# Performance work log

Measured on AMD Instinct MI355X. Metric: run time of the kernel, lower is better.

The kernel has to match this reference:

```python
import jax, jax.numpy as jnp
import numpy as np

B, C, H, W = 64, 512, 32, 32
D = C // 8  # 64


def setup_inputs() -> dict:
    key = jax.random.key(0)
    k1, k2, k3, k4 = jax.random.split(key, 4)
    x = jax.random.normal(k1, (B, C, H, W), dtype=jnp.float32)
    query_m = jax.random.normal(k2, (H * W, D), dtype=jnp.float32)
    key_m = jax.random.normal(k3, (H * W, D), dtype=jnp.float32)
    # 1x1 conv C->C: weight [C_out, C_in], kaiming-ish scale
    value_w = jax.random.normal(k4, (C, C), dtype=jnp.float32) * (1.0 / np.sqrt(C))
    value_b = jnp.zeros((C,), dtype=jnp.float32)
    return {"x": x, "query_m": query_m, "key_m": key_m,
            "value_w": value_w, "value_b": value_b}


def reference(x, query_m, key_m, value_w, value_b):
    b, c, h, w = x.shape
    xf = x.reshape(b, c, h * w)                        # [B, C, N]
    q = jnp.einsum('bcn,nd->bcd', xf, query_m)         # [B, C, D]
    k = jnp.einsum('bcn,nd->bcd', xf, key_m)           # [B, C, D]
    energy = jnp.einsum('bcd,bed->bce', q, k)          # [B, C, C]
    energy = jax.nn.sigmoid(energy)
    attention = jax.nn.softmax(energy, axis=-2)        # softmax over rows (dim=-2)
    # 1x1 conv = channel matmul + bias
    v = jnp.einsum('bcn,oc->bon', xf, value_w) + value_b[None, :, None]  # [B, C, N]
    # out[b,j,n] = sum_i v[b,i,n] * attention[b,i,j]
    out = jnp.einsum('bin,bij->bjn', v, attention)     # [B, C, N]
    return out.reshape(b, c, h, w)
```

## Files before the change

kernel.cpp:

```cpp
#include <hip/hip_runtime.h>

#define BK 32

typedef __attribute__((ext_vector_type(8))) short bf16x8;
typedef __attribute__((ext_vector_type(4))) float f32x4;

__device__ __forceinline__ unsigned short f2bf(float f) {
  unsigned u = __builtin_bit_cast(unsigned, f);
  unsigned r = (u + 0x7FFFu + ((u >> 16) & 1u)) >> 16;
  return (unsigned short)r;
}
__device__ __forceinline__ float bf2f(unsigned short h) {
  return __builtin_bit_cast(float, (unsigned)h << 16);
}
__device__ __forceinline__ unsigned pack2(unsigned short a, unsigned short b) {
  return (unsigned)a | ((unsigned)b << 16);
}

__device__ __forceinline__ void gld_lds16(const void* g, void* l) {
  __builtin_amdgcn_global_load_lds(
      (const __attribute__((address_space(1))) unsigned int*)g,
      (__attribute__((address_space(3))) unsigned int*)l, 16, 0, 0);
}

#define SCHED0() __builtin_amdgcn_sched_barrier(0)
#define NTBAR() do { SCHED0(); __builtin_amdgcn_s_barrier(); SCHED0(); } while (0)
#define VMW(N) do { asm volatile("s_waitcnt vmcnt(" #N ")" ::: "memory"); SCHED0(); } while (0)
#define LGKM0() do { asm volatile("s_waitcnt lgkmcnt(0)" ::: "memory"); SCHED0(); } while (0)
#define MFMA16(a, b, c) __builtin_amdgcn_mfma_f32_16x16x32_bf16(a, b, c, 0, 0, 0)

__device__ __forceinline__ void split8_store(float4 v0, float4 v1,
                                             unsigned short* Hdst,
                                             unsigned short* Ldst) {
  float f[8] = {v0.x, v0.y, v0.z, v0.w, v1.x, v1.y, v1.z, v1.w};
  unsigned short hh[8], ll[8];
#pragma unroll
  for (int i = 0; i < 8; ++i) {
    hh[i] = f2bf(f[i]);
    ll[i] = f2bf(f[i] - bf2f(hh[i]));
  }
  *reinterpret_cast<uint4*>(Hdst) = make_uint4(pack2(hh[0], hh[1]), pack2(hh[2], hh[3]),
                                               pack2(hh[4], hh[5]), pack2(hh[6], hh[7]));
  *reinterpret_cast<uint4*>(Ldst) = make_uint4(pack2(ll[0], ll[1]), pack2(ll[2], ll[3]),
                                               pack2(ll[4], ll[5]), pack2(ll[6], ll[7]));
}

__device__ __forceinline__ void split8_store_tt(float4 v0, float4 v1,
                                                unsigned short* Hdst,
                                                unsigned short* Ldst,
                                                unsigned short* Ttb,
                                                int kslot, int c) {
  float f[8] = {v0.x, v0.y, v0.z, v0.w, v1.x, v1.y, v1.z, v1.w};
  unsigned short hh[8], ll[8];
#pragma unroll
  for (int i = 0; i < 8; ++i) {
    hh[i] = f2bf(f[i]);
    ll[i] = f2bf(f[i] - bf2f(hh[i]));
  }
  *reinterpret_cast<uint4*>(Hdst) = make_uint4(pack2(hh[0], hh[1]), pack2(hh[2], hh[3]),
                                               pack2(hh[4], hh[5]), pack2(hh[6], hh[7]));
  *reinterpret_cast<uint4*>(Ldst) = make_uint4(pack2(ll[0], ll[1]), pack2(ll[2], ll[3]),
                                               pack2(ll[4], ll[5]), pack2(ll[6], ll[7]));
#pragma unroll
  for (int i = 0; i < 8; ++i) {
    int g = ((c >> 3) ^ i ^ kslot) & 7;
    Ttb[(kslot * 8 + i) * 72 + g * 8 + (c & 7)] = hh[i];
  }
}

__global__ __launch_bounds__(256) void qkm_split(const float* __restrict__ Qm,
                                                 const float* __restrict__ Km,
                                                 unsigned short* __restrict__ Th,
                                                 unsigned short* __restrict__ Tl) {
  __shared__ float lt[64][65];
  int k0 = blockIdx.x * 64;
  int half = blockIdx.y;
  const float* M = half ? Km : Qm;
  int t = threadIdx.x;
  int cl = (t & 15) * 4;
  int rl = t >> 4;
#pragma unroll
  for (int rr = 0; rr < 4; ++rr) {
    int r = rl + rr * 16;
    float4 v = *reinterpret_cast<const float4*>(&M[(long)(k0 + r) * 64 + cl]);
    lt[cl + 0][r] = v.x;
    lt[cl + 1][r] = v.y;
    lt[cl + 2][r] = v.z;
    lt[cl + 3][r] = v.w;
  }
  __syncthreads();
#pragma unroll
  for (int rr = 0; rr < 4; ++rr) {
    int c = rl + rr * 16;
    unsigned short h[4], lo[4];
#pragma unroll
    for (int i = 0; i < 4; ++i) {
      float f = lt[c][cl + i];
      h[i] = f2bf(f);
      lo[i] = f2bf(f - bf2f(h[i]));
    }
    *reinterpret_cast<uint2*>(&Th[(long)(half * 64 + c) * 1024 + k0 + cl]) =
        make_uint2(pack2(h[0], h[1]), pack2(h[2], h[3]));
    *reinterpret_cast<uint2*>(&Tl[(long)(half * 64 + c) * 1024 + k0 + cl]) =
        make_uint2(pack2(lo[0], lo[1]), pack2(lo[2], lo[3]));
  }
}

__global__ __launch_bounds__(256) void k1_mfma(const float* __restrict__ x,
                                               const unsigned short* __restrict__ Th,
                                               const unsigned short* __restrict__ Tl,
                                               unsigned short* __restrict__ qkh,
                                               unsigned short* __restrict__ qkl,
                                               unsigned short* __restrict__ xbT) {
  __shared__ unsigned short Dh[2][128 * 32];
  __shared__ unsigned short Dl[2][128 * 32];
  __shared__ unsigned short Xh[2][64 * 32];
  __shared__ unsigned short Xl[2][64 * 32];
  __shared__ unsigned short Tt[2][32 * 72];
  const int t = threadIdx.x;
  const int l = t & 63;
  const int w = t >> 6;
  const int wr = w >> 1, wc = w & 1;
  const long mBase = (long)blockIdx.x * 64;
  const int b = blockIdx.x >> 3;
  const int cBase = (blockIdx.x & 7) * 64;

  f32x4 acc[4][2];
#pragma unroll
  for (int m = 0; m < 4; ++m)
#pragma unroll
    for (int n = 0; n < 2; ++n) acc[m][n] = (f32x4){0.f, 0.f, 0.f, 0.f};

  const int xrow_l = t >> 2;
  const int kslot = t & 3;
  const int xsl = kslot ^ ((t >> 3) & 3);
  const int srcslot = (l & 3) ^ ((l >> 3) & 3);
  const int frag_off = (l & 15) * 32 + ((((l >> 4) ^ (l >> 1)) & 3) * 8);
  const float* xrow = x + (mBase + xrow_l) * 1024;

#define K1_STAGE_B(k0, p)                                                     \
  {                                                                           \
    _Pragma("unroll") for (int c = 0; c < 2; ++c) {                           \
      int ch = c * 4 + w;                                                     \
      int row = ch * 16 + (l >> 2);                                           \
      gld_lds16(Th + (long)row * 1024 + (k0) + srcslot * 8, &Dh[p][ch * 512]);\
      gld_lds16(Tl + (long)row * 1024 + (k0) + srcslot * 8, &Dl[p][ch * 512]);\
    }                                                                         \
  }

#define K1_COMPUTE(p)                                                         \
  {                                                                           \
    bf16x8 dh[4], dl[4], xh[2], xl[2];                                        \
    _Pragma("unroll") for (int m = 0; m < 4; ++m) {                           \
      dh[m] = *reinterpret_cast<const bf16x8*>(&Dh[p][(wr * 64 + m * 16) * 32 + frag_off]); \
      dl[m] = *reinterpret_cast<const bf16x8*>(&Dl[p][(wr * 64 + m * 16) * 32 + frag_off]); \
    }                                                                         \
    _Pragma("unroll") for (int n = 0; n < 2; ++n) {                           \
      xh[n] = *reinterpret_cast<const bf16x8*>(&Xh[p][(wc * 32 + n * 16) * 32 + frag_off]); \
      xl[n] = *reinterpret_cast<const bf16x8*>(&Xl[p][(wc * 32 + n * 16) * 32 + frag_off]); \
    }                                                                         \
    _Pragma("unroll") for (int m = 0; m < 4; ++m)                             \
        _Pragma("unroll") for (int n = 0; n < 2; ++n) {                       \
      acc[m][n] = MFMA16(dh[m], xh[n], acc[m][n]);                            \
      acc[m][n] = MFMA16(dh[m], xl[n], acc[m][n]);                            \
      acc[m][n] = MFMA16(dl[m], xh[n], acc[m][n]);                            \
    }                                                                         \
  }

#define K1_WRITEBACK(p, kk)                                                   \
  {                                                                           \
    int n2 = t >> 3;                                                          \
    int g2 = t & 7;                                                           \
    int gs = (g2 ^ (n2 & 7) ^ (n2 >> 3)) & 7;                                 \
    uint4 vv = *reinterpret_cast<const uint4*>(&Tt[p][n2 * 72 + gs * 8]);     \
    *reinterpret_cast<uint4*>(                                                \
        &xbT[(long)b * 524288 + (long)((kk) + n2) * 512 + cBase + g2 * 8]) = vv; \
  }

  {
    float4 p0 = *reinterpret_cast<const float4*>(&xrow[kslot * 8]);
    float4 p1 = *reinterpret_cast<const float4*>(&xrow[kslot * 8 + 4]);
    K1_STAGE_B(0, 0);
    split8_store_tt(p0, p1, &Xh[0][xrow_l * 32 + xsl * 8], &Xl[0][xrow_l * 32 + xsl * 8],
                    Tt[0], kslot, xrow_l);
  }

  for (int k0 = 0; k0 < 1024; k0 += 64) {
    __syncthreads();
    float4 na0 = *reinterpret_cast<const float4*>(&xrow[k0 + 32 + kslot * 8]);
    float4 na1 = *reinterpret_cast<const float4*>(&xrow[k0 + 32 + kslot * 8 + 4]);
    K1_STAGE_B(k0 + 32, 1);
    K1_COMPUTE(0);
    split8_store_tt(na0, na1, &Xh[1][xrow_l * 32 + xsl * 8], &Xl[1][xrow_l * 32 + xsl * 8],
                    Tt[1], kslot, xrow_l);
    K1_WRITEBACK(0, k0);
    __syncthreads();
    if (k0 + 64 < 1024) {
      float4 nb0 = *reinterpret_cast<const float4*>(&xrow[k0 + 64 + kslot * 8]);
      float4 nb1 = *reinterpret_cast<const float4*>(&xrow[k0 + 64 + kslot * 8 + 4]);
      K1_STAGE_B(k0 + 64, 0);
      K1_COMPUTE(1);
      split8_store_tt(nb0, nb1, &Xh[0][xrow_l * 32 + xsl * 8], &Xl[0][xrow_l * 32 + xsl * 8],
                      Tt[0], kslot, xrow_l);
      K1_WRITEBACK(1, k0 + 32);
    } else {
      K1_COMPUTE(1);
      K1_WRITEBACK(1, k0 + 32);
    }
  }

#pragma unroll
  for (int m = 0; m < 4; ++m)
#pragma unroll
    for (int n = 0; n < 2; ++n) {
      int d0 = wr * 64 + m * 16 + (l >> 4) * 4;
      long xr = mBase + wc * 32 + n * 16 + (l & 15);
      unsigned short h4[4], l4[4];
#pragma unroll
      for (int reg = 0; reg < 4; ++reg) {
        float v = acc[m][n][reg];
        h4[reg] = f2bf(v);
        l4[reg] = f2bf(v - bf2f(h4[reg]));
      }
      *reinterpret_cast<uint2*>(&qkh[xr * 128 + d0]) =
          make_uint2(pack2(h4[0], h4[1]), pack2(h4[2], h4[3]));
      *reinterpret_cast<uint2*>(&qkl[xr * 128 + d0]) =
          make_uint2(pack2(l4[0], l4[1]), pack2(l4[2], l4[3]));
    }
#undef K1_STAGE_B
#undef K1_COMPUTE
#undef K1_WRITEBACK
}

__global__ __launch_bounds__(256) void k2a_mfma(const unsigned short* __restrict__ qkh,
                                                const unsigned short* __restrict__ qkl,
                                                unsigned short* __restrict__ st) {
  __shared__ unsigned short Ah[128 * 64];
  __shared__ unsigned short Al[128 * 64];
  __shared__ unsigned short Bh[128 * 64];
  __shared__ unsigned short Bl[128 * 64];
  const int t = threadIdx.x;
  const int l = t & 63;
  const int w = t >> 6;
  const int wr = w >> 1, wc = w & 1;

  const int cpx = gridDim.x >> 3;
  const int orig = blockIdx.x;
  const int lw = (orig & 7) * cpx + (orig >> 3);
  const int b = lw >> 4;
  const int tile = lw & 15;
  const int iBase = (tile >> 2) * 128;
  const int jBase = (tile & 3) * 128;
  const long bq = (long)b * 512;

  const int sg = (l & 7) ^ (l >> 3);
#pragma unroll
  for (int c4 = 0; c4 < 4; ++c4) {
    int rb = w * 32 + c4 * 8;
    long rowA = bq + iBase + rb + (l >> 3);
    long rowB = bq + jBase + rb + (l >> 3);
    gld_lds16(qkh + rowA * 128 + sg * 8, &Ah[rb * 64]);
    gld_lds16(qkl + rowA * 128 + sg * 8, &Al[rb * 64]);
    gld_lds16(qkh + rowB * 128 + 64 + sg * 8, &Bh[rb * 64]);
    gld_lds16(qkl + rowB * 128 + 64 + sg * 8, &Bl[rb * 64]);
  }
  __syncthreads();

  f32x4 acc[4][4];
#pragma unroll
  for (int m = 0; m < 4; ++m)
#pragma unroll
    for (int n = 0; n < 4; ++n) acc[m][n] = (f32x4){0.f, 0.f, 0.f, 0.f};

#pragma unroll
  for (int ks = 0; ks < 2; ++ks) {
    bf16x8 ah[4], al4[4], bh[4], bl4[4];
#pragma unroll
    for (int m = 0; m < 4; ++m) {
      int row = wr * 64 + m * 16 + (l & 15);
      int off = row * 64 + ((ks * 4 + (l >> 4)) ^ (row & 7)) * 8;
      ah[m] = *reinterpret_cast<const bf16x8*>(&Ah[off]);
      al4[m] = *reinterpret_cast<const bf16x8*>(&Al[off]);
    }
#pragma unroll
    for (int n = 0; n < 4; ++n) {
      int row = wc * 64 + n * 16 + (l & 15);
      int off = row * 64 + ((ks * 4 + (l >> 4)) ^ (row & 7)) * 8;
      bh[n] = *reinterpret_cast<const bf16x8*>(&Bh[off]);
      bl4[n] = *reinterpret_cast<const bf16x8*>(&Bl[off]);
    }
#pragma unroll
    for (int m = 0; m < 4; ++m)
#pragma unroll
      for (int n = 0; n < 4; ++n) {
        acc[m][n] = MFMA16(ah[m], bh[n], acc[m][n]);
        acc[m][n] = MFMA16(ah[m], bl4[n], acc[m][n]);
        acc[m][n] = MFMA16(al4[m], bh[n], acc[m][n]);
      }
  }

  unsigned short* sb = st + (long)b * 512 * 512;
#pragma unroll
  for (int m = 0; m < 4; ++m)
#pragma unroll
    for (int n = 0; n < 4; ++n) {
      int i0 = iBase + wr * 64 + m * 16 + (l >> 4) * 4;
      int j = jBase + wc * 64 + n * 16 + (l & 15);
      unsigned short p[4];
#pragma unroll
      for (int reg = 0; reg < 4; ++reg) {
        float sg2 = 1.0f / (1.0f + __expf(-acc[m][n][reg]));
        p[reg] = f2bf(__expf(sg2));
      }
      *reinterpret_cast<uint2*>(&sb[(long)j * 512 + i0]) = *reinterpret_cast<uint2*>(p);
    }
}

__global__ __launch_bounds__(256) void k2b_rsum(const unsigned short* __restrict__ st,
                                                const float* __restrict__ bias,
                                                float* __restrict__ rsum,
                                                float* __restrict__ attbias) {
  int jg = blockIdx.x * 4 + (threadIdx.x >> 6);
  int l = threadIdx.x & 63;
  const unsigned short* row = st + (long)jg * 512 + l * 8;
  ushort4 u0 = *reinterpret_cast<const ushort4*>(row);
  ushort4 u1 = *reinterpret_cast<const ushort4*>(row + 4);
  float4 b0 = *reinterpret_cast<const float4*>(&bias[l * 8]);
  float4 b1 = *reinterpret_cast<const float4*>(&bias[l * 8 + 4]);
  float f0 = bf2f(u0.x), f1 = bf2f(u0.y), f2 = bf2f(u0.z), f3 = bf2f(u0.w);
  float f4 = bf2f(u1.x), f5 = bf2f(u1.y), f6 = bf2f(u1.z), f7 = bf2f(u1.w);
  float sum = (f0 + f1) + (f2 + f3) + ((f4 + f5) + (f6 + f7));
  float sumb = f0 * b0.x + f1 * b0.y + f2 * b0.z + f3 * b0.w +
               f4 * b1.x + f5 * b1.y + f6 * b1.z + f7 * b1.w;
#pragma unroll
  for (int off = 32; off > 0; off >>= 1) {
    sum += __shfl_down(sum, off);
    sumb += __shfl_down(sumb, off);
  }
  if (l == 0) {
    float r = 1.0f / sum;
    rsum[jg] = r;
    attbias[jg] = sumb * r;
  }
}

__global__ __launch_bounds__(256) void transpose_conv(const float* __restrict__ in,
                                                      unsigned short* __restrict__ out,
                                                      int inRows, int inCols,
                                                      long inBatch, long outBatch) {
  __shared__ unsigned short lt[64][65];
  int b = blockIdx.z;
  int r0 = blockIdx.y * 64;
  int c0 = blockIdx.x * 64;
  const float* I = in + (long)b * inBatch;
  unsigned short* O = out + (long)b * outBatch;
  int t = threadIdx.x;
  int cl = (t & 15) * 4;
  int rl = t >> 4;
#pragma unroll
  for (int rr = 0; rr < 4; ++rr) {
    int r = rl + rr * 16;
    float4 v = *reinterpret_cast<const float4*>(&I[(long)(r0 + r) * inCols + c0 + cl]);
    lt[cl + 0][r] = f2bf(v.x);
    lt[cl + 1][r] = f2bf(v.y);
    lt[cl + 2][r] = f2bf(v.z);
    lt[cl + 3][r] = f2bf(v.w);
  }
  __syncthreads();
#pragma unroll
  for (int rr = 0; rr < 4; ++rr) {
    int c = rl + rr * 16;
    unsigned short v[4] = {lt[c][cl], lt[c][cl + 1], lt[c][cl + 2], lt[c][cl + 3]};
    *reinterpret_cast<uint2*>(&O[(long)(c0 + c) * inRows + r0 + cl]) =
        *reinterpret_cast<uint2*>(&v[0]);
  }
}

template <int MODE>
__global__ __launch_bounds__(512) void mfma_nt256(const unsigned short* __restrict__ Abase,
                                                  const unsigned short* __restrict__ Bbase,
                                                  const float* __restrict__ rowscale,
                                                  unsigned short* __restrict__ Wout,
                                                  float* __restrict__ Fout) {
  __shared__ unsigned short As[2][256 * 64];
  __shared__ unsigned short Bs[2][256 * 64];
  const int t = threadIdx.x;
  const int l = t & 63;
  const int w = t >> 6;
  const int wr = w >> 2;
  const int wc = w & 3;

  const int cpx = gridDim.x >> 3;
  const int orig = blockIdx.x;
  const int lw = (orig & 7) * cpx + (orig >> 3);
  const int TPB_SH = (MODE == 0) ? 2 : 3;
  const int b = lw >> TPB_SH;
  const int tile = lw & ((1 << TPB_SH) - 1);
  const int mBase = (tile >> 1) * 256;
  const int nBase = (tile & 1) * 256;

  const unsigned short* Ag = Abase + ((MODE == 0) ? 0L : (long)b * (1024 * 512)) + (long)mBase * 512;
  const unsigned short* Bg = Bbase + (long)b * (512 * 512) + (long)nBase * 512;

  f32x4 acc[8][4];
#pragma unroll
  for (int m = 0; m < 8; ++m)
#pragma unroll
    for (int n = 0; n < 4; ++n) acc[m][n] = (f32x4){0.f, 0.f, 0.f, 0.f};

  const int srcslot = (l & 7) ^ (l >> 3);
  const int so0 = ((l >> 4) ^ (l & 7)) * 8;
  const int so1 = ((4 + (l >> 4)) ^ (l & 7)) * 8;

#define STG_A(p, tt, pr)                                                       \
  gld_lds16(Ag + (long)((pr) * 64 + w * 8 + (l >> 3)) * 512 + (tt) * 64 + srcslot * 8, \
            &As[p][((pr) * 64 + w * 8) * 64]);
#define STG_B(p, tt, pr)                                                       \
  gld_lds16(Bg + (long)((pr) * 64 + w * 8 + (l >> 3)) * 512 + (tt) * 64 + srcslot * 8, \
            &Bs[p][((pr) * 64 + w * 8) * 64]);

#define PHASE(p, q, STAGE_STMT, VMSTMT)                                        \
  {                                                                            \
    bf16x8 a00 = *reinterpret_cast<const bf16x8*>(                             \
        &As[p][(wr * 128 + (2 * (q)) * 16 + (l & 15)) * 64 + so0]);            \
    bf16x8 a01 = *reinterpret_cast<const bf16x8*>(                             \
        &As[p][(wr * 128 + (2 * (q)) * 16 + (l & 15)) * 64 + so1]);            \
    bf16x8 a10 = *reinterpret_cast<const bf16x8*>(                             \
        &As[p][(wr * 128 + (2 * (q) + 1) * 16 + (l & 15)) * 64 + so0]);        \
    bf16x8 a11 = *reinterpret_cast<const bf16x8*>(                             \
        &As[p][(wr * 128 + (2 * (q) + 1) * 16 + (l & 15)) * 64 + so1]);        \
    if ((q) == 0) {                                                            \
      _Pragma("unroll") for (int n = 0; n < 4; ++n) {                          \
        bfr0[n] = *reinterpret_cast<const bf16x8*>(                            \
            &Bs[p][(wc * 64 + n * 16 + (l & 15)) * 64 + so0]);                 \
        bfr1[n] = *reinterpret_cast<const bf16x8*>(                            \
            &Bs[p][(wc * 64 + n * 16 + (l & 15)) * 64 + so1]);                 \
      }                                                                        \
    }                                                                          \
    STAGE_STMT;                                                                \
    SCHED0();                                                                  \
    __builtin_amdgcn_s_barrier();                                              \
    LGKM0();                                                                   \
    __builtin_amdgcn_s_setprio(1);                                             \
    _Pragma("unroll") for (int n = 0; n < 4; ++n) {                            \
      acc[2 * (q)][n] = MFMA16(a00, bfr0[n], acc[2 * (q)][n]);                 \
      acc[2 * (q)][n] = MFMA16(a01, bfr1[n], acc[2 * (q)][n]);                 \
      acc[2 * (q) + 1][n] = MFMA16(a10, bfr0[n], acc[2 * (q) + 1][n]);         \
      acc[2 * (q) + 1][n] = MFMA16(a11, bfr1[n], acc[2 * (q) + 1][n]);         \
    }                                                                          \
    __builtin_amdgcn_s_setprio(0);                                             \
    VMSTMT;                                                                    \
    NTBAR();                                                                   \
  }

  bf16x8 bfr0[4], bfr1[4];

  STG_A(0, 0, 0); STG_A(0, 0, 1); STG_A(0, 0, 2); STG_A(0, 0, 3);
  STG_B(0, 0, 0); STG_B(0, 0, 1); STG_B(0, 0, 2); STG_B(0, 0, 3);
  STG_B(1, 1, 0); STG_B(1, 1, 1); STG_B(1, 1, 2); STG_B(1, 1, 3);
  STG_A(1, 1, 0); STG_A(1, 1, 2);
  VMW(6);
  NTBAR();

  for (int it = 0; it < 4; ++it) {
    const int t1 = 2 * it + 1;
    const int t2 = (2 * it + 2 < 8) ? 2 * it + 2 : 7;
    const int t3 = (2 * it + 3 < 8) ? 2 * it + 3 : 7;
    PHASE(0, 0, { STG_A(1, t1, 1); STG_A(1, t1, 3); }, );
    PHASE(0, 1, { STG_B(0, t2, 0); STG_B(0, t2, 1); }, VMW(10));
    PHASE(0, 2, { STG_B(0, t2, 2); STG_B(0, t2, 3); }, );
    PHASE(0, 3, { STG_A(0, t2, 0); STG_A(0, t2, 2); }, VMW(8));
    PHASE(1, 0, { STG_A(0, t2, 1); STG_A(0, t2, 3); }, );
    PHASE(1, 1, { STG_B(1, t3, 0); STG_B(1, t3, 1); }, VMW(10));
    PHASE(1, 2, { STG_B(1, t3, 2); STG_B(1, t3, 3); }, );
    PHASE(1, 3, { STG_A(1, t3, 0); STG_A(1, t3, 2); }, VMW(8));
  }
#undef PHASE
#undef STG_A
#undef STG_B

  if (MODE == 0) {
    unsigned short* W = Wout + (long)b * (512 * 512);
#pragma unroll
    for (int n = 0; n < 4; ++n) {
      int j = nBase + wc * 64 + n * 16 + (l & 15);
      float rs = rowscale[b * 512 + j];
#pragma unroll
      for (int m = 0; m < 8; ++m) {
        int c0 = mBase + wr * 128 + m * 16 + (l >> 4) * 4;
        unsigned short p[4];
#pragma unroll
        for (int reg = 0; reg < 4; ++reg) p[reg] = f2bf(acc[m][n][reg] * rs);
        *reinterpret_cast<uint2*>(&W[(long)j * 512 + c0]) = *reinterpret_cast<uint2*>(p);
      }
    }
  } else {
    float* O = Fout + (long)b * (512 * 1024);
#pragma unroll
    for (int n = 0; n < 4; ++n) {
      int j = nBase + wc * 64 + n * 16 + (l & 15);
      float ab = rowscale[b * 512 + j];
#pragma unroll
      for (int m = 0; m < 8; ++m) {
        int n0 = mBase + wr * 128 + m * 16 + (l >> 4) * 4;
        *reinterpret_cast<float4*>(&O[(long)j * 1024 + n0]) =
            make_float4(acc[m][n][0] + ab, acc[m][n][1] + ab,
                        acc[m][n][2] + ab, acc[m][n][3] + ab);
      }
    }
  }
}

extern "C" void kernel_launch(void* const* d_in, const int* in_sizes, int n_in,
                              void* d_out, int out_size, void* d_ws, size_t ws_size,
                              hipStream_t stream) {
  const float* x  = (const float*)d_in[0];
  const float* Qm = (const float*)d_in[1];
  const float* Km = (const float*)d_in[2];
  const float* vw = (const float*)d_in[3];
  const float* vb = (const float*)d_in[4];
  float* out = (float*)d_out;

  float* ws = (float*)d_ws;
  unsigned short* qkh  = (unsigned short*)ws;
  unsigned short* qkl  = qkh + 4194304;
  unsigned short* st   = (unsigned short*)(ws + 4194304);
  unsigned short* weff = (unsigned short*)(ws + 4194304 + 8388608);
  unsigned short* xbT  = (unsigned short*)(ws + 4194304 + 16777216);
  unsigned short* vwT  = (unsigned short*)(ws + 4194304 + 33554432);
  unsigned short* qkTh = (unsigned short*)(ws + 4194304 + 33554432 + 131072);
  unsigned short* qkTl = qkTh + 131072;
  float* rsum    = ws + 4194304 + 33554432 + 131072 + 131072;
  float* attbias = rsum + 32768;

  transpose_conv<<<dim3(8, 8, 1), 256, 0, stream>>>(vw, vwT, 512, 512, 0L, 0L);
  qkm_split<<<dim3(16, 2), 256, 0, stream>>>(Qm, Km, qkTh, qkTl);
  k1_mfma<<<512, 256, 0, stream>>>(x, qkTh, qkTl, qkh, qkl, xbT);
  k2a_mfma<<<1024, 256, 0, stream>>>(qkh, qkl, st);
  k2b_rsum<<<8192, 256, 0, stream>>>(st, vb, rsum, attbias);
  mfma_nt256<0><<<256, 512, 0, stream>>>(vwT, st, rsum, weff, nullptr);
  mfma_nt256<1><<<512, 512, 0, stream>>>(xbT, weff, attbias, nullptr, out);
}
```

Measured before the change: 201.3 us.

## Restructure k1 main loop with register prefetch and explicit waitcnt barriers

The first kernel's K loop is rewritten so the x tile for step k+2 is loaded into registers one stage ahead, and the async LDS loads of the D tiles are issued after compute. Explicit vmcnt/lgkmcnt waits replace plain __syncthreads, so global loads can stay in flight across barriers. The aim is to hide global-load latency behind MFMA work. The cost is more registers in use and subtle ordering needs; the tail clamps the prefetch index to 31, which causes redundant loads on the last steps.

```diff
diff --git a/kernel.cpp b/kernel.cpp
--- a/kernel.cpp
+++ b/kernel.cpp
@@ -138,13 +138,19 @@
   const int frag_off = (l & 15) * 32 + ((((l >> 4) ^ (l >> 1)) & 3) * 8);
   const float* xrow = x + (mBase + xrow_l) * 1024;
 
-#define K1_STAGE_B(k0, p)                                                     \
+#define K1_LOADX(r0, r1, tt)                                                  \
+  {                                                                           \
+    r0 = *reinterpret_cast<const float4*>(&xrow[(tt) * 32 + kslot * 8]);      \
+    r1 = *reinterpret_cast<const float4*>(&xrow[(tt) * 32 + kslot * 8 + 4]);  \
+  }
+
+#define K1_STAGE_D(tt, p)                                                     \
   {                                                                           \
     _Pragma("unroll") for (int c = 0; c < 2; ++c) {                           \
       int ch = c * 4 + w;                                                     \
       int row = ch * 16 + (l >> 2);                                           \
-      gld_lds16(Th + (long)row * 1024 + (k0) + srcslot * 8, &Dh[p][ch * 512]);\
-      gld_lds16(Tl + (long)row * 1024 + (k0) + srcslot * 8, &Dl[p][ch * 512]);\
+      gld_lds16(Th + (long)row * 1024 + (tt) * 32 + srcslot * 8, &Dh[p][ch * 512]); \
+      gld_lds16(Tl + (long)row * 1024 + (tt) * 32 + srcslot * 8, &Dl[p][ch * 512]); \
     }                                                                         \
   }
 
@@ -177,35 +183,44 @@
         &xbT[(long)b * 524288 + (long)((kk) + n2) * 512 + cBase + g2 * 8]) = vv; \
   }
 
-  {
-    float4 p0 = *reinterpret_cast<const float4*>(&xrow[kslot * 8]);
-    float4 p1 = *reinterpret_cast<const float4*>(&xrow[kslot * 8 + 4]);
-    K1_STAGE_B(0, 0);
-    split8_store_tt(p0, p1, &Xh[0][xrow_l * 32 + xsl * 8], &Xl[0][xrow_l * 32 + xsl * 8],
-                    Tt[0], kslot, xrow_l);
-  }
-
-  for (int k0 = 0; k0 < 1024; k0 += 64) {
-    __syncthreads();
-    float4 na0 = *reinterpret_cast<const float4*>(&xrow[k0 + 32 + kslot * 8]);
-    float4 na1 = *reinterpret_cast<const float4*>(&xrow[k0 + 32 + kslot * 8 + 4]);
-    K1_STAGE_B(k0 + 32, 1);
-    K1_COMPUTE(0);
-    split8_store_tt(na0, na1, &Xh[1][xrow_l * 32 + xsl * 8], &Xl[1][xrow_l * 32 + xsl * 8],
-                    Tt[1], kslot, xrow_l);
-    K1_WRITEBACK(0, k0);
-    __syncthreads();
-    if (k0 + 64 < 1024) {
-      float4 nb0 = *reinterpret_cast<const float4*>(&xrow[k0 + 64 + kslot * 8]);
-      float4 nb1 = *reinterpret_cast<const float4*>(&xrow[k0 + 64 + kslot * 8 + 4]);
-      K1_STAGE_B(k0 + 64, 0);
+  float4 xa0, xa1, xb0, xb1;
+
+  K1_LOADX(xa0, xa1, 0);
+  K1_STAGE_D(0, 0);
+  K1_LOADX(xb0, xb1, 1);
+  split8_store_tt(xa0, xa1, &Xh[0][xrow_l * 32 + xsl * 8], &Xl[0][xrow_l * 32 + xsl * 8],
+                  Tt[0], kslot, xrow_l);
+  K1_STAGE_D(1, 1);
+  VMW(6);
+  LGKM0();
+  NTBAR();
+
+  for (int kt = 0; kt < 32; kt += 2) {
+    {
+      const int tn = (kt + 2 < 32) ? kt + 2 : 31;
+      K1_COMPUTE(0);
+      K1_WRITEBACK(0, kt * 32);
+      K1_LOADX(xa0, xa1, tn);
+      split8_store_tt(xb0, xb1, &Xh[1][xrow_l * 32 + xsl * 8], &Xl[1][xrow_l * 32 + xsl * 8],
+                      Tt[1], kslot, xrow_l);
+      LGKM0();
+      NTBAR();
+      K1_STAGE_D(tn, 0);
+      VMW(7);
+      NTBAR();
+    }
+    {
+      const int tn = (kt + 3 < 32) ? kt + 3 : 31;
       K1_COMPUTE(1);
-      split8_store_tt(nb0, nb1, &Xh[0][xrow_l * 32 + xsl * 8], &Xl[0][xrow_l * 32 + xsl * 8],
+      K1_WRITEBACK(1, (kt + 1) * 32);
+      K1_LOADX(xb0, xb1, tn);
+      split8_store_tt(xa0, xa1, &Xh[0][xrow_l * 32 + xsl * 8], &Xl[0][xrow_l * 32 + xsl * 8],
                       Tt[0], kslot, xrow_l);
-      K1_WRITEBACK(1, k0 + 32);
-    } else {
-      K1_COMPUTE(1);
-      K1_WRITEBACK(1, k0 + 32);
+      LGKM0();
+      NTBAR();
+      K1_STAGE_D(tn, 1);
+      VMW(7);
+      NTBAR();
     }
   }
 
@@ -227,7 +242,8 @@
       *reinterpret_cast<uint2*>(&qkl[xr * 128 + d0]) =
           make_uint2(pack2(l4[0], l4[1]), pack2(l4[2], l4[3]));
     }
-#undef K1_STAGE_B
+#undef K1_LOADX
+#undef K1_STAGE_D
 #undef K1_COMPUTE
 #undef K1_WRITEBACK
 }
```

Result: faster. 190.4 us (-5.4%).
